# Kernel tuning notes

Measured on AMD Instinct MI355X. Metric: run time of the kernel, lower is better.

Reference implementation:

```python
import jax, jax.numpy as jnp
import numpy as np

S_MIN = 0.01
S_MAX = 36500.0
SEQ_LEN = 128
BATCH = 65536


def setup_inputs() -> dict:
    key = jax.random.key(0)
    k1, k2 = jax.random.split(key)
    # elapsed days: nonnegative floats; ratings: integers 1..4 stored as float
    t = jax.random.uniform(k1, (SEQ_LEN, BATCH), dtype=jnp.float32) * 30.0
    rating = jax.random.randint(k2, (SEQ_LEN, BATCH), 1, 5).astype(jnp.float32)
    inputs = jnp.stack([t, rating], axis=-1)  # [S, B, 2]
    w = jnp.array([0.4, 0.6, 2.4, 5.8, 4.93, 0.94, 0.86, 0.01, 1.49,
                   0.14, 0.94, 2.18, 0.05, 0.34, 1.26, 0.29, 2.61],
                  dtype=jnp.float32)
    return {"inputs": inputs, "w": w}


def _first_step(X, w):
    # state is all-zeros only on the first step (clamp keeps s >= S_MIN after)
    rating = X[:, 1]
    ridx = jnp.clip(rating.astype(jnp.int32) - 1, 0, 3)
    valid = (rating >= 1) & (rating <= 4)
    new_s = jnp.where(valid, w[ridx], 1.0)
    new_d = jnp.clip(w[4] - w[5] * (rating - 3.0), 1.0, 10.0)
    new_s = jnp.clip(new_s, S_MIN, S_MAX)
    return jnp.stack([new_s, new_d], axis=1)  # [B, 2]


def _step(w, state, X):
    s, d = state[:, 0], state[:, 1]
    t, rating = X[:, 0], X[:, 1]
    # power forgetting curve: r = (1 + t / (9 s))^-1
    r = 1.0 / (1.0 + t / (9.0 * s))
    hard_penalty = jnp.where(rating == 2, w[15], 1.0)
    easy_bonus = jnp.where(rating == 4, w[16], 1.0)
    s_success = s * (1.0 + jnp.exp(w[8]) * (11.0 - d) * jnp.power(s, -w[9])
                     * (jnp.exp((1.0 - r) * w[10]) - 1.0)
                     * hard_penalty * easy_bonus)
    s_failure = jnp.minimum(
        w[11] * jnp.power(d, -w[12]) * (jnp.power(s + 1.0, w[13]) - 1.0)
        * jnp.exp((1.0 - r) * w[14]),
        s)
    new_s = jnp.where(rating > 1.0, s_success, s_failure)
    new_d = d - w[6] * (rating - 3.0)
    new_d = w[7] * w[4] + (1.0 - w[7]) * new_d  # mean reversion to w[4]
    new_d = jnp.clip(new_d, 1.0, 10.0)
    new_s = jnp.clip(new_s, S_MIN, S_MAX)
    new_state = jnp.stack([new_s, new_d], axis=1)
    return new_state, new_state


def reference(inputs, w):
    state0 = _first_step(inputs[0], w)  # [B, 2]
    final_state, rest = jax.lax.scan(lambda st, X: _step(w, st, X),
                                     state0, inputs[1:])
    outputs = jnp.concatenate([state0[None], rest], axis=0)  # [S, B, 2]
    return outputs, final_state
```

## Files before the change

### kernel.cpp

```cpp
#include <hip/hip_runtime.h>

#define BATCH_N 65536
#define SEQ_N   128

typedef float v2f __attribute__((ext_vector_type(2)));

__global__ __launch_bounds__(256) void fsrs_kernel(
    const v2f* __restrict__ in,
    const float* __restrict__ w,
    v2f*       __restrict__ out)
{
    const int b = blockIdx.x * 256 + threadIdx.x;

    const float w0 = w[0], w1 = w[1], w2 = w[2], w3 = w[3];
    const float w4 = w[4], w5 = w[5], w6 = w[6], w7 = w[7];
    const float w9 = w[9], w11 = w[11], w12 = w[12], w13 = w[13];
    const float w15 = w[15], w16 = w[16];
    constexpr float LOG2E = 1.44269504088896340736f;
    const float w8l  = w[8]  * LOG2E;
    const float w10l = w[10] * LOG2E;
    const float w14l = w[14] * LOG2E;
    const float omw7   = 1.0f - w7;
    const float omw7w6 = omw7 * w6;
    const float dc0    = w7 * w4 + 3.0f * omw7w6;

    const v2f* ip = in  + b;
    v2f*       op = out + b;

    float s = 0.01f;
    float dcur = 1.0f;
    float dpre = 1.0f;

    v2f rawA[16], rawB[16];
    float tA[16], dA[16], mA[16];
    float tB[16], dB[16], mB[16];

    auto loadC = [&](v2f* raw, int base) {
#pragma unroll
        for (int i = 0; i < 16; ++i) raw[i] = ip[(base + i) * BATCH_N];
    };

    auto preC = [&](const v2f* raw, float* T, float* D, float* M, int lo) {
#pragma unroll
        for (int i = 0; i < 16; ++i) {
            if (i < lo) continue;
            const float tt = raw[i].x, rating = raw[i].y;
            const float hb = (rating == 2.0f) ? w15
                           : ((rating == 4.0f) ? w16 : 1.0f);
            const float eh = (11.0f - dpre) * hb;
            const float m2 = w11 * __builtin_amdgcn_exp2f(
                                 -w12 * __builtin_amdgcn_logf(dpre));
            M[i] = (rating > 1.0f) ? eh : -m2;
            const float nd = __builtin_fmaf(omw7, dpre,
                              __builtin_fmaf(-omw7w6, rating, dc0));
            dpre = fminf(fmaxf(nd, 1.0f), 10.0f);
            T[i] = tt;
            D[i] = dpre;
        }
    };

    auto stepC = [&](const float* T, const float* D, const float* M,
                     int base, int lo) {
#pragma unroll
        for (int i = 0; i < 16; ++i) {
            if (i < lo) continue;
            const float tt = T[i], ms = M[i];
            const bool  sel = ms > 0.0f;
            const float q   = __builtin_fmaf(9.0f, s, tt);
            const float omr = tt * __builtin_amdgcn_rcpf(q);
            const float e   = __builtin_amdgcn_exp2f(omr * (sel ? w10l : w14l));
            const float a1  = __builtin_fmaf(-w9, __builtin_amdgcn_logf(s), w8l);
            const float a2  = w13 * __builtin_amdgcn_logf(s + 1.0f);
            const float A   = __builtin_amdgcn_exp2f(sel ? a1 : a2);
            const float Af  = sel ? A          : (A - 1.0f);
            const float Ef  = sel ? (e - 1.0f) : e;
            const float m   = sel ? (ms * s)   : (-ms);
            const float P   = Af * Ef * m;
            const float ns  = sel ? (s + P) : fminf(P, s);
            s = fminf(fmaxf(ns, 0.01f), 36500.0f);
            dcur = D[i];
            v2f o; o.x = s; o.y = dcur;
            __builtin_nontemporal_store(o, &op[(base + i) * BATCH_N]);
        }
    };

    loadC(rawA, 0);
    {
        const float rating = rawA[0].y;
        const float d0 = fminf(fmaxf(w4 - w5 * (rating - 3.0f), 1.0f), 10.0f);
        dpre = d0;
        tA[0] = rawA[0].x; dA[0] = d0; mA[0] = 1.0f;
    }
    preC(rawA, tA, dA, mA, 1);

    loadC(rawB, 16);
    {
        const float rating = rawA[0].y;
        const float wsel = (rating < 2.5f) ? ((rating < 1.5f) ? w0 : w1)
                                           : ((rating < 3.5f) ? w2 : w3);
        const float ns = (rating >= 1.0f && rating <= 4.0f) ? wsel : 1.0f;
        s = fminf(fmaxf(ns, 0.01f), 36500.0f);
        dcur = dA[0];
        v2f o; o.x = s; o.y = dcur;
        __builtin_nontemporal_store(o, &op[0]);
    }
    stepC(tA, dA, mA, 0, 1);
    preC(rawB, tB, dB, mB, 0);

#pragma unroll 1
    for (int c = 0; c < 3; ++c) {
        loadC(rawA, 32 * c + 32);
        stepC(tB, dB, mB, 32 * c + 16, 0);
        preC(rawA, tA, dA, mA, 0);

        loadC(rawB, 32 * c + 48);
        stepC(tA, dA, mA, 32 * c + 32, 0);
        preC(rawB, tB, dB, mB, 0);
    }

    stepC(tB, dB, mB, 112, 0);

    {
        v2f o; o.x = s; o.y = dcur;
        op[SEQ_N * BATCH_N] = o;
    }
}

extern "C" void kernel_launch(void* const* d_in, const int* in_sizes, int n_in,
                              void* d_out, int out_size, void* d_ws, size_t ws_size,
                              hipStream_t stream) {
    const v2f*   in = (const v2f*)d_in[0];
    const float* w  = (const float*)d_in[1];
    v2f* out = (v2f*)d_out;
    fsrs_kernel<<<BATCH_N / 256, 256, 0, stream>>>(in, w, out);
}
```

Measured before the change: 117.3 us.

## Deepen load prefetch pipeline and merge success/failure log paths in recurrence

```diff
diff --git a/kernel.cpp b/kernel.cpp
--- a/kernel.cpp
+++ b/kernel.cpp
@@ -5,7 +5,7 @@
 
 typedef float v2f __attribute__((ext_vector_type(2)));
 
-__global__ __launch_bounds__(256) void fsrs_kernel(
+__global__ __launch_bounds__(256, 1) void fsrs_kernel(
     const v2f* __restrict__ in,
     const float* __restrict__ w,
     v2f*       __restrict__ out)
@@ -28,7 +28,6 @@
     v2f*       op = out + b;
 
     float s = 0.01f;
-    float dcur = 1.0f;
     float dpre = 1.0f;
 
     v2f rawA[16], rawB[16];
@@ -69,59 +68,64 @@
             const float q   = __builtin_fmaf(9.0f, s, tt);
             const float omr = tt * __builtin_amdgcn_rcpf(q);
             const float e   = __builtin_amdgcn_exp2f(omr * (sel ? w10l : w14l));
-            const float a1  = __builtin_fmaf(-w9, __builtin_amdgcn_logf(s), w8l);
-            const float a2  = w13 * __builtin_amdgcn_logf(s + 1.0f);
-            const float A   = __builtin_amdgcn_exp2f(sel ? a1 : a2);
+            const float ls  = __builtin_amdgcn_logf(sel ? s : (s + 1.0f));
+            const float aa  = sel ? __builtin_fmaf(-w9, ls, w8l) : (w13 * ls);
+            const float A   = __builtin_amdgcn_exp2f(aa);
             const float Af  = sel ? A          : (A - 1.0f);
             const float Ef  = sel ? (e - 1.0f) : e;
             const float m   = sel ? (ms * s)   : (-ms);
             const float P   = Af * Ef * m;
-            const float ns  = sel ? (s + P) : fminf(P, s);
-            s = fminf(fmaxf(ns, 0.01f), 36500.0f);
-            dcur = D[i];
-            v2f o; o.x = s; o.y = dcur;
+            const float su  = fminf(s + P, 36500.0f);
+            const float fl  = fmaxf(fminf(P, s), 0.01f);
+            s = sel ? su : fl;
+            v2f o; o.x = s; o.y = D[i];
             __builtin_nontemporal_store(o, &op[(base + i) * BATCH_N]);
         }
     };
 
     loadC(rawA, 0);
+    loadC(rawB, 16);
+
+    const float t0 = rawA[0].x, r0 = rawA[0].y;
     {
-        const float rating = rawA[0].y;
-        const float d0 = fminf(fmaxf(w4 - w5 * (rating - 3.0f), 1.0f), 10.0f);
+        const float d0 = fminf(fmaxf(
+            __builtin_fmaf(-w5, r0 - 3.0f, w4), 1.0f), 10.0f);
         dpre = d0;
-        tA[0] = rawA[0].x; dA[0] = d0; mA[0] = 1.0f;
+        tA[0] = t0; dA[0] = d0; mA[0] = 1.0f;
     }
     preC(rawA, tA, dA, mA, 1);
+    loadC(rawA, 32);
 
-    loadC(rawB, 16);
     {
-        const float rating = rawA[0].y;
-        const float wsel = (rating < 2.5f) ? ((rating < 1.5f) ? w0 : w1)
-                                           : ((rating < 3.5f) ? w2 : w3);
-        const float ns = (rating >= 1.0f && rating <= 4.0f) ? wsel : 1.0f;
+        const float wsel = (r0 < 2.5f) ? ((r0 < 1.5f) ? w0 : w1)
+                                       : ((r0 < 3.5f) ? w2 : w3);
+        const float ns = (r0 >= 1.0f && r0 <= 4.0f) ? wsel : 1.0f;
         s = fminf(fmaxf(ns, 0.01f), 36500.0f);
-        dcur = dA[0];
-        v2f o; o.x = s; o.y = dcur;
+        v2f o; o.x = s; o.y = dA[0];
         __builtin_nontemporal_store(o, &op[0]);
     }
     stepC(tA, dA, mA, 0, 1);
     preC(rawB, tB, dB, mB, 0);
+    loadC(rawB, 48);
 
 #pragma unroll 1
-    for (int c = 0; c < 3; ++c) {
-        loadC(rawA, 32 * c + 32);
-        stepC(tB, dB, mB, 32 * c + 16, 0);
+    for (int c = 0; c < 2; ++c) {
+        stepC(tB, dB, mB, 16 + 32 * c, 0);
         preC(rawA, tA, dA, mA, 0);
-
-        loadC(rawB, 32 * c + 48);
-        stepC(tA, dA, mA, 32 * c + 32, 0);
+        loadC(rawA, 64 + 32 * c);
+        stepC(tA, dA, mA, 32 + 32 * c, 0);
         preC(rawB, tB, dB, mB, 0);
+        loadC(rawB, 80 + 32 * c);
     }
 
+    stepC(tB, dB, mB, 80, 0);
+    preC(rawA, tA, dA, mA, 0);
+    stepC(tA, dA, mA, 96, 0);
+    preC(rawB, tB, dB, mB, 0);
     stepC(tB, dB, mB, 112, 0);
 
     {
-        v2f o; o.x = s; o.y = dcur;
+        v2f o; o.x = s; o.y = dB[15];
         op[SEQ_N * BATCH_N] = o;
     }
 }
```

Measured after the change: 115.0 us. No clear change (-1.9%).
